# Optimization experiments

Hardware: AMD Instinct MI355X
Metric: run time of the kernel (lower is better)

The kernel has to match this reference:

```python
import jax, jax.numpy as jnp
import numpy as np

# Static problem dims (match input_specs)
B, N, C, H, W = 1, 3, 128, 256, 256
HEADS = 4
# _compute_dynamic_scales(256,256) with max_attention_size=4096:
# min_scale = max(2, int(sqrt(65536/4096))) = 4 -> scales [4,8,16], sorted desc:
SCALES = [16, 8, 4]


def setup_inputs() -> dict:
    key = jax.random.key(0)
    ks = jax.random.split(key, 8)
    S = len(SCALES)
    std = 0.05  # small init to keep logits in a sane range
    return {
        "query": jax.random.normal(ks[0], (B, C, H, W), jnp.float32),
        "keys": jax.random.normal(ks[1], (B, N, C, H, W), jnp.float32),
        "values": jax.random.normal(ks[2], (B, N, C, H, W), jnp.float32),
        "wq": jax.random.normal(ks[3], (S, C, C), jnp.float32) * std,
        "bq": jnp.zeros((S, C), jnp.float32),
        "wk": jax.random.normal(ks[4], (S, C, C), jnp.float32) * std,
        "bk": jnp.zeros((S, C), jnp.float32),
        "wv": jax.random.normal(ks[5], (S, C, C), jnp.float32) * std,
        "bv": jnp.zeros((S, C), jnp.float32),
        "fusion_w": jax.random.normal(ks[6], (C, 3 * C), jnp.float32) * std,
        "fusion_b": jnp.zeros((C,), jnp.float32),
        "out_w": jax.random.normal(ks[7], (C, C), jnp.float32) * std,
        "out_b": jnp.zeros((C,), jnp.float32),
    }


def _pool(x, s):
    """Average pool by integer factor s over the last two dims (adaptive_avg_pool2d
    with divisible sizes)."""
    *lead, c, h, w = x.shape
    return x.reshape(*lead, c, h // s, s, w // s, s).mean(axis=(-3, -1))


def _conv1x1(x, w, b):
    # x: [..., C_in, H, W], w: [C_out, C_in], b: [C_out]
    y = jnp.einsum('...chw,oc->...ohw', x, w)
    return y + b.reshape((1,) * (y.ndim - 3) + (-1, 1, 1))


def reference(query, keys, values, wq, bq, wk, bk, wv, bv,
              fusion_w, fusion_b, out_w, out_b):
    hd = C // HEADS
    outs = []
    for si, s in enumerate(SCALES):
        Hs, Ws = H // s, W // s
        L = Hs * Ws
        q_s = _pool(query, s)   # [B,C,Hs,Ws]
        k_s = _pool(keys, s)    # [B,N,C,Hs,Ws]
        v_s = _pool(values, s)  # [B,N,C,Hs,Ws]
        q = _conv1x1(q_s, wq[si], bq[si])
        k = _conv1x1(k_s, wk[si], bk[si])
        v = _conv1x1(v_s, wv[si], bv[si])
        q = q.reshape(B, HEADS, hd, L).transpose(0, 1, 3, 2)       # [B,h,L,d]
        k = k.reshape(B, N, HEADS, hd, L)                          # [B,N,h,d,M]
        v = v.reshape(B, N, HEADS, hd, L).transpose(0, 1, 2, 4, 3) # [B,N,h,M,d]
        scores = jnp.einsum('bhld,bnhdm->bnhlm', q, k) * (hd ** -0.5)
        attn = jax.nn.softmax(scores, axis=-1)                      # stable softmax
        out = jnp.einsum('bnhlm,bnhmd->bnhld', attn, v).mean(axis=1)  # mean over anchors
        out = out.transpose(0, 1, 3, 2).reshape(B, C, Hs, Ws)
        if s > 1:
            # F.interpolate bilinear, align_corners=False (half-pixel centers)
            out = jax.image.resize(out, (B, C, H, W), method='bilinear')
        outs.append(out)
    fused = jnp.concatenate(outs, axis=1)  # [B, 3C, H, W]
    y = _conv1x1(fused, fusion_w, fusion_b)
    return _conv1x1(y, out_w, out_b)
```

## Files before the change

### kernel.cpp

```cpp
#include <hip/hip_runtime.h>
#include <hip/hip_bf16.h>


typedef __attribute__((ext_vector_type(8))) short bf16x8;
typedef __attribute__((ext_vector_type(4))) float f32x4;

__device__ inline ushort rne_bf16(float x) {
  uint u = __float_as_uint(x);
  return (ushort)((u + 0x7fffu + ((u >> 16) & 1u)) >> 16);
}

__device__ inline uint pk2_bf16(float a, float b) {
  float2 f2; f2.x = a; f2.y = b;
  __hip_bfloat162 h = __float22bfloat162_rn(f2);
  union { __hip_bfloat162 h; uint u; } cvt; cvt.h = h;
  return cvt.u;
}

__global__ __launch_bounds__(256) void pool4_kernel(
    const float* __restrict__ query, const float* __restrict__ keys,
    const float* __restrict__ values, float* __restrict__ out)
{
  int idx = blockIdx.x * 256 + threadIdx.x;
  int x = idx & 63, y = (idx >> 6) & 63, mc = idx >> 12;
  int map = mc >> 7, c = mc & 127;
  const float* src;
  if (map == 0)      src = query  + (size_t)c * 65536;
  else if (map <= 3) src = keys   + (size_t)((map - 1) * 128 + c) * 65536;
  else               src = values + (size_t)((map - 4) * 128 + c) * 65536;
  src += (y * 4) * 256 + x * 4;
  float s = 0.f;
#pragma unroll
  for (int r = 0; r < 4; ++r) {
    float4 v = *(const float4*)(src + r * 256);
    s += v.x + v.y + v.z + v.w;
  }
  out[idx] = s * 0.0625f;
}

__global__ __launch_bounds__(256) void pool2_kernel(
    const float* __restrict__ in, float* __restrict__ out, int hw)
{
  int idx = blockIdx.x * 256 + threadIdx.x;
  int x = idx % hw; int y = (idx / hw) % hw; int mc = idx / (hw * hw);
  int w2 = hw * 2;
  const float* s = in + (size_t)mc * w2 * w2 + (2 * y) * w2 + 2 * x;
  float2 a = *(const float2*)s;
  float2 b = *(const float2*)(s + w2);
  out[idx] = (a.x + a.y + b.x + b.y) * 0.25f;
}

__global__ __launch_bounds__(256) void precomp_kernel(
    const float* __restrict__ fusion_w, const float* __restrict__ fusion_b,
    const float* __restrict__ out_w, const float* __restrict__ out_b,
    float* __restrict__ Wc, float* __restrict__ bc)
{
  int idx = blockIdx.x * 256 + threadIdx.x;
  if (idx < 128 * 384) {
    int o = idx / 384, k = idx % 384;
    float s = 0.f;
    for (int c = 0; c < 128; ++c)
      s = fmaf(out_w[o * 128 + c], fusion_w[c * 384 + k], s);
    Wc[idx] = s;
  } else if (idx < 128 * 384 + 128) {
    int o = idx - 128 * 384;
    float s = out_b[o];
    for (int c = 0; c < 128; ++c)
      s = fmaf(out_w[o * 128 + c], fusion_b[c], s);
    bc[o] = s;
  }
}

__global__ __launch_bounds__(256) void proj_kernel(
    const float* __restrict__ pooled,
    ushort* __restrict__ qb, ushort* __restrict__ kbb, ushort* __restrict__ vbb,
    const float* __restrict__ wq, const float* __restrict__ bq,
    const float* __restrict__ wk, const float* __restrict__ bk,
    const float* __restrict__ wv, const float* __restrict__ bv,
    int si, int L, float qscale)
{
  __shared__ float Wt[32][68];
  __shared__ float Xs[32][64];
  int map = blockIdx.z;
  int o0 = blockIdx.y * 64;
  int l0 = blockIdx.x * 64;
  const float* w; const float* b; float sc = 1.f;
  if (map == 0)      { w = wq + si * 16384; b = bq + si * 128; sc = qscale; }
  else if (map <= 3) { w = wk + si * 16384; b = bk + si * 128; }
  else               { w = wv + si * 16384; b = bv + si * 128; }
  const float* src = pooled + (size_t)map * 128 * L;
  int t = threadIdx.x;
  int og = t >> 4, lg = t & 15;
  float acc[4][4] = {};
  for (int c0 = 0; c0 < 128; c0 += 32) {
    __syncthreads();
    {
      int o = t >> 2, ci = (t & 3) * 8;
      const float* wp = w + (o0 + o) * 128 + c0 + ci;
      float4 a = *(const float4*)wp, d = *(const float4*)(wp + 4);
      Wt[ci + 0][o] = a.x; Wt[ci + 1][o] = a.y; Wt[ci + 2][o] = a.z; Wt[ci + 3][o] = a.w;
      Wt[ci + 4][o] = d.x; Wt[ci + 5][o] = d.y; Wt[ci + 6][o] = d.z; Wt[ci + 7][o] = d.w;
    }
    {
      int c = t >> 3, li = (t & 7) * 8;
      const float* xp = src + (size_t)(c0 + c) * L + l0 + li;
      float4 a = *(const float4*)xp, d = *(const float4*)(xp + 4);
      *(float4*)&Xs[c][li] = a; *(float4*)&Xs[c][li + 4] = d;
    }
    __syncthreads();
#pragma unroll 8
    for (int k = 0; k < 32; ++k) {
      float4 wv4 = *(const float4*)&Wt[k][4 * og];
      float4 xv4 = *(const float4*)&Xs[k][4 * lg];
      float wa[4] = {wv4.x, wv4.y, wv4.z, wv4.w};
      float xa[4] = {xv4.x, xv4.y, xv4.z, xv4.w};
#pragma unroll
      for (int r = 0; r < 4; ++r)
#pragma unroll
        for (int c = 0; c < 4; ++c)
          acc[r][c] = fmaf(wa[r], xa[c], acc[r][c]);
    }
  }
  float4 b4 = *(const float4*)&b[o0 + 4 * og];
  float ba[4] = {b4.x, b4.y, b4.z, b4.w};
  if (map < 4) {
    ushort* dst = (map == 0) ? qb : (kbb + (size_t)(map - 1) * L * 32 * 4);
    int o4 = o0 + 4 * og;
    size_t hbase = (size_t)(o4 >> 5) * L * 32 + (o4 & 31);
#pragma unroll
    for (int li = 0; li < 4; ++li) {
      ushort4 r;
      r.x = rne_bf16((acc[0][li] + ba[0]) * sc);
      r.y = rne_bf16((acc[1][li] + ba[1]) * sc);
      r.z = rne_bf16((acc[2][li] + ba[2]) * sc);
      r.w = rne_bf16((acc[3][li] + ba[3]) * sc);
      *(ushort4*)&dst[hbase + (size_t)(l0 + 4 * lg + li) * 32] = r;
    }
  } else {
    ushort* dst = vbb + (size_t)(map - 4) * 128 * L;
    int m = l0 + 4 * lg;
#pragma unroll
    for (int oi = 0; oi < 4; ++oi) {
      int o = o0 + 4 * og + oi;
      int h = o >> 5, d = o & 31;
      ushort4 r;
      r.x = rne_bf16(acc[oi][0] + ba[oi]);
      r.y = rne_bf16(acc[oi][1] + ba[oi]);
      r.z = rne_bf16(acc[oi][2] + ba[oi]);
      r.w = rne_bf16(acc[oi][3] + ba[oi]);
      size_t off = (size_t)h * 32 * L
                 + ((size_t)(m >> 5) * 2 + (d >> 4)) * 512
                 + (size_t)(d & 15) * 32 + ((m >> 3) & 3) * 8 + (m & 7);
      *(ushort4*)&dst[off] = r;
    }
  }
}

#define PSTR 72
__global__ __launch_bounds__(256, 4) void attn_mfma_kernel(
    const ushort* __restrict__ qb, const ushort* __restrict__ kb,
    const ushort* __restrict__ vb, float* __restrict__ onp,
    float* __restrict__ lsp, int L, int msplit)
{
  __shared__ __align__(16) ushort P[2][4][2][16][PSTR];
  int t = threadIdx.x;
  int wave = t >> 6, lane = t & 63;
  int col = lane & 15, quad = lane >> 4;
  int head = blockIdx.y;
  int anchor = blockIdx.z / msplit, mpart = blockIdx.z % msplit;
  int l = blockIdx.x * 128 + wave * 32;
  int mlen = L / msplit, mbase = mpart * mlen;
  int ntile = mlen >> 6;

  const ushort* qh = qb + (size_t)head * L * 32;
  const ushort* kh = kb + ((size_t)anchor * 4 + head) * L * 32;
  const ushort* vh = vb + ((size_t)anchor * 4 + head) * 32 * L;

  bf16x8 qfA = *(const bf16x8*)(qh + (size_t)(l + col) * 32 + quad * 8);
  bf16x8 qfB = *(const bf16x8*)(qh + (size_t)(l + 16 + col) * 32 + quad * 8);
  const ushort* kbase = kh + (size_t)mbase * 32 + col * 32 + quad * 8;
  const ushort* vbase = vh + (size_t)(mbase >> 5) * 1024 + col * 32 + quad * 8;

  f32x4 odA0 = {0.f,0.f,0.f,0.f}, odA1 = {0.f,0.f,0.f,0.f};
  f32x4 odB0 = {0.f,0.f,0.f,0.f}, odB1 = {0.f,0.f,0.f,0.f};
  f32x4 lsaA = {0.f,0.f,0.f,0.f}, lsaB = {0.f,0.f,0.f,0.f};
  const f32x4 z = {0.f,0.f,0.f,0.f};
  const bf16x8 ones = {16256,16256,16256,16256,16256,16256,16256,16256};

  ushort* Pa = &P[0][wave][0][0][0];
  ushort* Pb = &P[1][wave][0][0][0];
  const int HOF = 16 * PSTR;

  auto expstore = [&](f32x4 a0, f32x4 a1, f32x4 a2, f32x4 a3, ushort* Pw) {
    float sv[4][4] = {{a0.x,a0.y,a0.z,a0.w},{a1.x,a1.y,a1.z,a1.w},
                      {a2.x,a2.y,a2.z,a2.w},{a3.x,a3.y,a3.z,a3.w}};
#pragma unroll
    for (int j = 0; j < 4; ++j) {
      uint u0 = pk2_bf16(__builtin_amdgcn_exp2f(sv[j][0]),
                         __builtin_amdgcn_exp2f(sv[j][1]));
      uint u1 = pk2_bf16(__builtin_amdgcn_exp2f(sv[j][2]),
                         __builtin_amdgcn_exp2f(sv[j][3]));
      uint2 dw; dw.x = u0; dw.y = u1;
      *(uint2*)&Pw[col * PSTR + 16 * j + quad * 4] = dw;
    }
  };

  bf16x8 k0 = *(const bf16x8*)(kbase);
  bf16x8 k1 = *(const bf16x8*)(kbase + 512);
  bf16x8 k2 = *(const bf16x8*)(kbase + 1024);
  bf16x8 k3 = *(const bf16x8*)(kbase + 1536);
  {
    f32x4 t0 = __builtin_amdgcn_mfma_f32_16x16x32_bf16(k0, qfA, z, 0, 0, 0);
    f32x4 t1 = __builtin_amdgcn_mfma_f32_16x16x32_bf16(k1, qfA, z, 0, 0, 0);
    f32x4 t2 = __builtin_amdgcn_mfma_f32_16x16x32_bf16(k2, qfA, z, 0, 0, 0);
    f32x4 t3 = __builtin_amdgcn_mfma_f32_16x16x32_bf16(k3, qfA, z, 0, 0, 0);
    expstore(t0, t1, t2, t3, Pa);
    t0 = __builtin_amdgcn_mfma_f32_16x16x32_bf16(k0, qfB, z, 0, 0, 0);
    t1 = __builtin_amdgcn_mfma_f32_16x16x32_bf16(k1, qfB, z, 0, 0, 0);
    t2 = __builtin_amdgcn_mfma_f32_16x16x32_bf16(k2, qfB, z, 0, 0, 0);
    t3 = __builtin_amdgcn_mfma_f32_16x16x32_bf16(k3, qfB, z, 0, 0, 0);
    const ushort* kp1 = kbase + ((ntile > 1) ? 64 * 32 : 0);
    k0 = *(const bf16x8*)(kp1);
    k1 = *(const bf16x8*)(kp1 + 512);
    k2 = *(const bf16x8*)(kp1 + 1024);
    k3 = *(const bf16x8*)(kp1 + 1536);
    expstore(t0, t1, t2, t3, Pa + HOF);
  }

  for (int i = 1; i < ntile; ++i) {
    const ushort* vpn = vbase + (i - 1) * 2048;
    bf16x8 vA = *(const bf16x8*)(vpn);
    bf16x8 vB = *(const bf16x8*)(vpn + 1024);
    bf16x8 vC = *(const bf16x8*)(vpn + 512);
    bf16x8 vD = *(const bf16x8*)(vpn + 1536);
    bf16x8 pA0 = *(const bf16x8*)(&Pa[col * PSTR + quad * 8]);
    bf16x8 pA1 = *(const bf16x8*)(&Pa[col * PSTR + 32 + quad * 8]);
    bf16x8 pB0 = *(const bf16x8*)(&Pa[HOF + col * PSTR + quad * 8]);
    bf16x8 pB1 = *(const bf16x8*)(&Pa[HOF + col * PSTR + 32 + quad * 8]);
    f32x4 t0 = __builtin_amdgcn_mfma_f32_16x16x32_bf16(k0, qfA, z, 0, 0, 0);
    f32x4 t1 = __builtin_amdgcn_mfma_f32_16x16x32_bf16(k1, qfA, z, 0, 0, 0);
    f32x4 t2 = __builtin_amdgcn_mfma_f32_16x16x32_bf16(k2, qfA, z, 0, 0, 0);
    f32x4 t3 = __builtin_amdgcn_mfma_f32_16x16x32_bf16(k3, qfA, z, 0, 0, 0);
    lsaA = __builtin_amdgcn_mfma_f32_16x16x32_bf16(pA0, ones, lsaA, 0, 0, 0);
    lsaA = __builtin_amdgcn_mfma_f32_16x16x32_bf16(pA1, ones, lsaA, 0, 0, 0);
    odA0 = __builtin_amdgcn_mfma_f32_16x16x32_bf16(pA0, vA, odA0, 0, 0, 0);
    odA0 = __builtin_amdgcn_mfma_f32_16x16x32_bf16(pA1, vB, odA0, 0, 0, 0);
    odA1 = __builtin_amdgcn_mfma_f32_16x16x32_bf16(pA0, vC, odA1, 0, 0, 0);
    odA1 = __builtin_amdgcn_mfma_f32_16x16x32_bf16(pA1, vD, odA1, 0, 0, 0);
    expstore(t0, t1, t2, t3, Pb);
    t0 = __builtin_amdgcn_mfma_f32_16x16x32_bf16(k0, qfB, z, 0, 0, 0);
    t1 = __builtin_amdgcn_mfma_f32_16x16x32_bf16(k1, qfB, z, 0, 0, 0);
    t2 = __builtin_amdgcn_mfma_f32_16x16x32_bf16(k2, qfB, z, 0, 0, 0);
    t3 = __builtin_amdgcn_mfma_f32_16x16x32_bf16(k3, qfB, z, 0, 0, 0);
    {
      const ushort* kpn = kbase + ((i + 1 < ntile) ? (i + 1) * 2048 : 0);
      k0 = *(const bf16x8*)(kpn);
      k1 = *(const bf16x8*)(kpn + 512);
      k2 = *(const bf16x8*)(kpn + 1024);
      k3 = *(const bf16x8*)(kpn + 1536);
    }
    lsaB = __builtin_amdgcn_mfma_f32_16x16x32_bf16(pB0, ones, lsaB, 0, 0, 0);
    lsaB = __builtin_amdgcn_mfma_f32_16x16x32_bf16(pB1, ones, lsaB, 0, 0, 0);
    odB0 = __builtin_amdgcn_mfma_f32_16x16x32_bf16(pB0, vA, odB0, 0, 0, 0);
    odB0 = __builtin_amdgcn_mfma_f32_16x16x32_bf16(pB1, vB, odB0, 0, 0, 0);
    odB1 = __builtin_amdgcn_mfma_f32_16x16x32_bf16(pB0, vC, odB1, 0, 0, 0);
    odB1 = __builtin_amdgcn_mfma_f32_16x16x32_bf16(pB1, vD, odB1, 0, 0, 0);
    expstore(t0, t1, t2, t3, Pb + HOF);
    ushort* tp = Pa; Pa = Pb; Pb = tp;
  }

  {
    const ushort* vpe = vbase + (ntile - 1) * 2048;
    bf16x8 vA = *(const bf16x8*)(vpe);
    bf16x8 vB = *(const bf16x8*)(vpe + 1024);
    bf16x8 vC = *(const bf16x8*)(vpe + 512);
    bf16x8 vD = *(const bf16x8*)(vpe + 1536);
    bf16x8 pA0 = *(const bf16x8*)(&Pa[col * PSTR + quad * 8]);
    bf16x8 pA1 = *(const bf16x8*)(&Pa[col * PSTR + 32 + quad * 8]);
    bf16x8 pB0 = *(const bf16x8*)(&Pa[HOF + col * PSTR + quad * 8]);
    bf16x8 pB1 = *(const bf16x8*)(&Pa[HOF + col * PSTR + 32 + quad * 8]);
    lsaA = __builtin_amdgcn_mfma_f32_16x16x32_bf16(pA0, ones, lsaA, 0, 0, 0);
    lsaA = __builtin_amdgcn_mfma_f32_16x16x32_bf16(pA1, ones, lsaA, 0, 0, 0);
    odA0 = __builtin_amdgcn_mfma_f32_16x16x32_bf16(pA0, vA, odA0, 0, 0, 0);
    odA0 = __builtin_amdgcn_mfma_f32_16x16x32_bf16(pA1, vB, odA0, 0, 0, 0);
    odA1 = __builtin_amdgcn_mfma_f32_16x16x32_bf16(pA0, vC, odA1, 0, 0, 0);
    odA1 = __builtin_amdgcn_mfma_f32_16x16x32_bf16(pA1, vD, odA1, 0, 0, 0);
    lsaB = __builtin_amdgcn_mfma_f32_16x16x32_bf16(pB0, ones, lsaB, 0, 0, 0);
    lsaB = __builtin_amdgcn_mfma_f32_16x16x32_bf16(pB1, ones, lsaB, 0, 0, 0);
    odB0 = __builtin_amdgcn_mfma_f32_16x16x32_bf16(pB0, vA, odB0, 0, 0, 0);
    odB0 = __builtin_amdgcn_mfma_f32_16x16x32_bf16(pB1, vB, odB0, 0, 0, 0);
    odB1 = __builtin_amdgcn_mfma_f32_16x16x32_bf16(pB0, vC, odB1, 0, 0, 0);
    odB1 = __builtin_amdgcn_mfma_f32_16x16x32_bf16(pB1, vD, odB1, 0, 0, 0);
  }

  float* on2 = onp + ((size_t)(mpart * 3 + anchor) * 128 + (size_t)(head * 32)) * L;
  float* ls2 = lsp + ((size_t)(mpart * 3 + anchor) * 4 + head) * L;
  if (col == 0) {
    *(f32x4*)&ls2[l + quad * 4] = lsaA;
    *(f32x4*)&ls2[l + 16 + quad * 4] = lsaB;
  }
  *(f32x4*)&on2[(size_t)col * L + l + quad * 4]             = odA0;
  *(f32x4*)&on2[(size_t)(16 + col) * L + l + quad * 4]      = odA1;
  *(f32x4*)&on2[(size_t)col * L + l + 16 + quad * 4]        = odB0;
  *(f32x4*)&on2[(size_t)(16 + col) * L + l + 16 + quad * 4] = odB1;
}

__global__ __launch_bounds__(256) void norm_kernel(
    const float* __restrict__ on4,  const float* __restrict__ ls4,  float* __restrict__ a4,
    const float* __restrict__ on8,  const float* __restrict__ ls8,  float* __restrict__ a8,
    const float* __restrict__ on16, const float* __restrict__ ls16, float* __restrict__ a16)
{
  int i = blockIdx.x * 256 + threadIdx.x;
  const float* on; const float* ls; float* ax; int L;
  if (i < 131072)      { on = on4;  ls = ls4;  ax = a4;  L = 4096; }
  else if (i < 163840) { i -= 131072; on = on8;  ls = ls8;  ax = a8;  L = 1024; }
  else                 { i -= 163840; on = on16; ls = ls16; ax = a16; L = 256; }
  int e = i * 4;
  int c = e / L, l = e % L;
  int h = c >> 5;
  float ax0 = 0.f, ax1 = 0.f, ax2 = 0.f, ax3 = 0.f;
  for (int a = 0; a < 3; ++a) {
    float n0 = 0.f, n1 = 0.f, n2 = 0.f, n3 = 0.f;
    float d0 = 0.f, d1 = 0.f, d2 = 0.f, d3 = 0.f;
#pragma unroll
    for (int mp = 0; mp < 2; ++mp) {
      int g = mp * 3 + a;
      float4 o = *(const float4*)&on[((size_t)g * 128 + c) * L + l];
      float4 s = *(const float4*)&ls[((size_t)g * 4 + h) * L + l];
      n0 += o.x; n1 += o.y; n2 += o.z; n3 += o.w;
      d0 += s.x; d1 += s.y; d2 += s.z; d3 += s.w;
    }
    ax0 += n0 / d0; ax1 += n1 / d1; ax2 += n2 / d2; ax3 += n3 / d3;
  }
  const float third = 1.f / 3.f;
  float4 r = make_float4(ax0 * third, ax1 * third, ax2 * third, ax3 * third);
  *(float4*)&ax[e] = r;
}

__global__ __launch_bounds__(256) void ygemm_kernel(
    const float* __restrict__ a16, const float* __restrict__ a8,
    const float* __restrict__ a4, const float* __restrict__ Wc,
    float* __restrict__ y16, float* __restrict__ y8, float* __restrict__ y4)
{
  __shared__ float Wt[32][68];
  __shared__ float Xs[32][64];
  int bx = blockIdx.x;
  int o0 = blockIdx.y * 64;
  int sci; int lt; const float* src; float* dst; int L;
  if (bx < 4)       { sci = 0; lt = bx;      src = a16; dst = y16; L = 256; }
  else if (bx < 20) { sci = 1; lt = bx - 4;  src = a8;  dst = y8;  L = 1024; }
  else              { sci = 2; lt = bx - 20; src = a4;  dst = y4;  L = 4096; }
  int l0 = lt * 64;
  int coff = sci * 128;
  int t = threadIdx.x;
  int og = t >> 4, lg = t & 15;
  float acc[4][4] = {};
  for (int c0 = 0; c0 < 128; c0 += 32) {
    __syncthreads();
    {
      int o = t >> 2, ci = (t & 3) * 8;
      const float* wp = Wc + (o0 + o) * 384 + coff + c0 + ci;
      float4 a = *(const float4*)wp, d = *(const float4*)(wp + 4);
      Wt[ci + 0][o] = a.x; Wt[ci + 1][o] = a.y; Wt[ci + 2][o] = a.z; Wt[ci + 3][o] = a.w;
      Wt[ci + 4][o] = d.x; Wt[ci + 5][o] = d.y; Wt[ci + 6][o] = d.z; Wt[ci + 7][o] = d.w;
    }
    {
      int c = t >> 3, li = (t & 7) * 8;
      const float* xp = src + (size_t)(c0 + c) * L + l0 + li;
      float4 a = *(const float4*)xp, d = *(const float4*)(xp + 4);
      *(float4*)&Xs[c][li] = a; *(float4*)&Xs[c][li + 4] = d;
    }
    __syncthreads();
#pragma unroll 8
    for (int k = 0; k < 32; ++k) {
      float4 wv4 = *(const float4*)&Wt[k][4 * og];
      float4 xv4 = *(const float4*)&Xs[k][4 * lg];
      float wa[4] = {wv4.x, wv4.y, wv4.z, wv4.w};
      float xa[4] = {xv4.x, xv4.y, xv4.z, xv4.w};
#pragma unroll
      for (int r = 0; r < 4; ++r)
#pragma unroll
        for (int c = 0; c < 4; ++c)
          acc[r][c] = fmaf(wa[r], xa[c], acc[r][c]);
    }
  }
#pragma unroll
  for (int r = 0; r < 4; ++r) {
    float4 v = make_float4(acc[r][0], acc[r][1], acc[r][2], acc[r][3]);
    *(float4*)&dst[(size_t)(o0 + 4 * og + r) * L + l0 + 4 * lg] = v;
  }
}

__device__ inline void add_bilinear(const float* __restrict__ Yrow0,
                                    const float* __restrict__ Yrow1,
                                    int ssz, float sf, float fy,
                                    int px0, float* r)
{
#pragma unroll
  for (int j = 0; j < 4; ++j) {
    float sx = (px0 + j + 0.5f) * sf - 0.5f;
    int xi = (int)floorf(sx);
    float fx = sx - xi;
    int x0 = max(xi, 0), x1 = min(xi + 1, ssz - 1);
    float a0 = Yrow0[x0], a1 = Yrow0[x1];
    float b0 = Yrow1[x0], b1 = Yrow1[x1];
    float v0 = a0 + fx * (a1 - a0);
    float v1 = b0 + fx * (b1 - b0);
    r[j] += v0 + fy * (v1 - v0);
  }
}

__global__ __launch_bounds__(256) void upsample_kernel(
    const float* __restrict__ y16, const float* __restrict__ y8,
    const float* __restrict__ y4, const float* __restrict__ bc,
    float* __restrict__ outp)
{
  int idx = blockIdx.x * 256 + threadIdx.x;
  int x4 = idx & 63, py = (idx >> 6) & 255, o = idx >> 14;
  int px0 = x4 * 4;
  float b = bc[o];
  float r[4] = {b, b, b, b};
#pragma unroll
  for (int s = 0; s < 3; ++s) {
    const float* Y; int ssz; float sf;
    if (s == 0)      { Y = y16; ssz = 16; sf = 1.f / 16.f; }
    else if (s == 1) { Y = y8;  ssz = 32; sf = 1.f / 8.f; }
    else             { Y = y4;  ssz = 64; sf = 1.f / 4.f; }
    const float* Yo = Y + (size_t)o * ssz * ssz;
    float sy = (py + 0.5f) * sf - 0.5f;
    int yi = (int)floorf(sy);
    float fy = sy - yi;
    int yy0 = max(yi, 0), yy1 = min(yi + 1, ssz - 1);
    add_bilinear(Yo + yy0 * ssz, Yo + yy1 * ssz, ssz, sf, fy, px0, r);
  }
  float4 v = make_float4(r[0], r[1], r[2], r[3]);
  *(float4*)&outp[(size_t)o * 65536 + py * 256 + px0] = v;
}

extern "C" void kernel_launch(void* const* d_in, const int* in_sizes, int n_in,
                              void* d_out, int out_size, void* d_ws, size_t ws_size,
                              hipStream_t stream) {
  const float* query    = (const float*)d_in[0];
  const float* keys     = (const float*)d_in[1];
  const float* values   = (const float*)d_in[2];
  const float* wq       = (const float*)d_in[3];
  const float* bq       = (const float*)d_in[4];
  const float* wk       = (const float*)d_in[5];
  const float* bk       = (const float*)d_in[6];
  const float* wv       = (const float*)d_in[7];
  const float* bv       = (const float*)d_in[8];
  const float* fusion_w = (const float*)d_in[9];
  const float* fusion_b = (const float*)d_in[10];
  const float* out_w    = (const float*)d_in[11];
  const float* out_b    = (const float*)d_in[12];
  float* wsf  = (float*)d_ws;
  float* outp = (float*)d_out;

  const size_t P4   = 0;
  const size_t P8   = 3670016;
  const size_t P16  = 4587520;
  const size_t ONP4  = 0;
  const size_t LSP4  = 3145728;
  const size_t ONP8  = 3244032;
  const size_t LSP8  = 4030464;
  const size_t ONP16 = 4055040;
  const size_t LSP16 = 4448256;
  const size_t Y4   = 0;
  const size_t Y8   = 524288;
  const size_t Y16  = 655360;
  const size_t QB4  = 4816896;
  const size_t KB4  = 5079040;
  const size_t VB4  = 5865472;
  const size_t QB8  = 6651904;
  const size_t KB8  = 6717440;
  const size_t VB8  = 6914048;
  const size_t QB16 = 7110656;
  const size_t KB16 = 7127040;
  const size_t VB16 = 7176192;
  const size_t A4   = 7225344;
  const size_t A8   = 7749632;
  const size_t A16  = 7880704;
  const size_t WC   = 7913472;
  const size_t BC   = 7962624;

  precomp_kernel<<<(128*384 + 128 + 255) / 256, 256, 0, stream>>>(
      fusion_w, fusion_b, out_w, out_b, wsf + WC, wsf + BC);
  pool4_kernel<<<7*128*4096/256, 256, 0, stream>>>(query, keys, values, wsf + P4);
  pool2_kernel<<<7*128*1024/256, 256, 0, stream>>>(wsf + P4, wsf + P8, 32);
  pool2_kernel<<<7*128*256/256,  256, 0, stream>>>(wsf + P8, wsf + P16, 16);

  const float qsc = 0.17677669529663687f * 1.4426950408889634f;
  proj_kernel<<<dim3(64, 2, 7), 256, 0, stream>>>(wsf + P4,
      (ushort*)(wsf + QB4), (ushort*)(wsf + KB4), (ushort*)(wsf + VB4),
      wq, bq, wk, bk, wv, bv, 2, 4096, qsc);
  proj_kernel<<<dim3(16, 2, 7), 256, 0, stream>>>(wsf + P8,
      (ushort*)(wsf + QB8), (ushort*)(wsf + KB8), (ushort*)(wsf + VB8),
      wq, bq, wk, bk, wv, bv, 1, 1024, qsc);
  proj_kernel<<<dim3(4, 2, 7), 256, 0, stream>>>(wsf + P16,
      (ushort*)(wsf + QB16), (ushort*)(wsf + KB16), (ushort*)(wsf + VB16),
      wq, bq, wk, bk, wv, bv, 0, 256, qsc);

  attn_mfma_kernel<<<dim3(32, 4, 6), 256, 0, stream>>>(
      (const ushort*)(wsf + QB4), (const ushort*)(wsf + KB4),
      (const ushort*)(wsf + VB4), wsf + ONP4, wsf + LSP4, 4096, 2);
  attn_mfma_kernel<<<dim3(8, 4, 6), 256, 0, stream>>>(
      (const ushort*)(wsf + QB8), (const ushort*)(wsf + KB8),
      (const ushort*)(wsf + VB8), wsf + ONP8, wsf + LSP8, 1024, 2);
  attn_mfma_kernel<<<dim3(2, 4, 6), 256, 0, stream>>>(
      (const ushort*)(wsf + QB16), (const ushort*)(wsf + KB16),
      (const ushort*)(wsf + VB16), wsf + ONP16, wsf + LSP16, 256, 2);

  norm_kernel<<<672, 256, 0, stream>>>(
      wsf + ONP4, wsf + LSP4, wsf + A4,
      wsf + ONP8, wsf + LSP8, wsf + A8,
      wsf + ONP16, wsf + LSP16, wsf + A16);

  ygemm_kernel<<<dim3(84, 2), 256, 0, stream>>>(
      wsf + A16, wsf + A8, wsf + A4, wsf + WC,
      wsf + Y16, wsf + Y8, wsf + Y4);
  upsample_kernel<<<8192, 256, 0, stream>>>(
      wsf + Y16, wsf + Y8, wsf + Y4, wsf + BC, outp);
}
```

Measured before the change: 414.1 us.

## Fuse three pooling levels into one kernel using wave shuffles

Replaces the 4x pooling kernel and the two 2x pooling kernels with one kernel where each thread averages a 16x4 strip into four 4x4-pooled outputs. It then uses lane shuffles to form the 8x and 16x pooled values. This removes two launches and the re-reading of intermediate pooled maps from memory. In exchange it has fewer threads, each doing more loads, and the row-strided access pattern may lower memory parallelism.

```diff
diff --git a/kernel.cpp b/kernel.cpp
--- a/kernel.cpp
+++ b/kernel.cpp
@@ -17,37 +17,63 @@
   return cvt.u;
 }
 
-__global__ __launch_bounds__(256) void pool4_kernel(
+__global__ __launch_bounds__(256) void pool_fused_kernel(
     const float* __restrict__ query, const float* __restrict__ keys,
-    const float* __restrict__ values, float* __restrict__ out)
+    const float* __restrict__ values, float* __restrict__ out4,
+    float* __restrict__ out8, float* __restrict__ out16)
 {
   int idx = blockIdx.x * 256 + threadIdx.x;
-  int x = idx & 63, y = (idx >> 6) & 63, mc = idx >> 12;
+  int x = idx & 63;
+  int t = (idx >> 6) & 15;
+  int mc = idx >> 10;
   int map = mc >> 7, c = mc & 127;
   const float* src;
   if (map == 0)      src = query  + (size_t)c * 65536;
   else if (map <= 3) src = keys   + (size_t)((map - 1) * 128 + c) * 65536;
   else               src = values + (size_t)((map - 4) * 128 + c) * 65536;
-  src += (y * 4) * 256 + x * 4;
-  float s = 0.f;
-#pragma unroll
-  for (int r = 0; r < 4; ++r) {
-    float4 v = *(const float4*)(src + r * 256);
-    s += v.x + v.y + v.z + v.w;
-  }
-  out[idx] = s * 0.0625f;
-}
-
-__global__ __launch_bounds__(256) void pool2_kernel(
-    const float* __restrict__ in, float* __restrict__ out, int hw)
-{
-  int idx = blockIdx.x * 256 + threadIdx.x;
-  int x = idx % hw; int y = (idx / hw) % hw; int mc = idx / (hw * hw);
-  int w2 = hw * 2;
-  const float* s = in + (size_t)mc * w2 * w2 + (2 * y) * w2 + 2 * x;
-  float2 a = *(const float2*)s;
-  float2 b = *(const float2*)(s + w2);
-  out[idx] = (a.x + a.y + b.x + b.y) * 0.25f;
+  src += (t * 16) * 256 + x * 4;
+
+  float4 v0  = *(const float4*)(src + 0 * 256);
+  float4 v1  = *(const float4*)(src + 1 * 256);
+  float4 v2  = *(const float4*)(src + 2 * 256);
+  float4 v3  = *(const float4*)(src + 3 * 256);
+  float4 v4  = *(const float4*)(src + 4 * 256);
+  float4 v5  = *(const float4*)(src + 5 * 256);
+  float4 v6  = *(const float4*)(src + 6 * 256);
+  float4 v7  = *(const float4*)(src + 7 * 256);
+  float4 v8  = *(const float4*)(src + 8 * 256);
+  float4 v9  = *(const float4*)(src + 9 * 256);
+  float4 v10 = *(const float4*)(src + 10 * 256);
+  float4 v11 = *(const float4*)(src + 11 * 256);
+  float4 v12 = *(const float4*)(src + 12 * 256);
+  float4 v13 = *(const float4*)(src + 13 * 256);
+  float4 v14 = *(const float4*)(src + 14 * 256);
+  float4 v15 = *(const float4*)(src + 15 * 256);
+
+  float s0 = ((v0.x + v0.y + v0.z + v0.w) + (v1.x + v1.y + v1.z + v1.w)
+            + (v2.x + v2.y + v2.z + v2.w) + (v3.x + v3.y + v3.z + v3.w)) * 0.0625f;
+  float s1 = ((v4.x + v4.y + v4.z + v4.w) + (v5.x + v5.y + v5.z + v5.w)
+            + (v6.x + v6.y + v6.z + v6.w) + (v7.x + v7.y + v7.z + v7.w)) * 0.0625f;
+  float s2 = ((v8.x + v8.y + v8.z + v8.w) + (v9.x + v9.y + v9.z + v9.w)
+            + (v10.x + v10.y + v10.z + v10.w) + (v11.x + v11.y + v11.z + v11.w)) * 0.0625f;
+  float s3 = ((v12.x + v12.y + v12.z + v12.w) + (v13.x + v13.y + v13.z + v13.w)
+            + (v14.x + v14.y + v14.z + v14.w) + (v15.x + v15.y + v15.z + v15.w)) * 0.0625f;
+
+  float* o4 = out4 + (size_t)mc * 4096 + (t * 4) * 64 + x;
+  o4[0] = s0; o4[64] = s1; o4[128] = s2; o4[192] = s3;
+
+  float s0p = __shfl_xor(s0, 1), s1p = __shfl_xor(s1, 1);
+  float s2p = __shfl_xor(s2, 1), s3p = __shfl_xor(s3, 1);
+  float e0 = ((s0 + s0p) + s1 + s1p) * 0.25f;
+  float e1 = ((s2 + s2p) + s3 + s3p) * 0.25f;
+  float e0q = __shfl_xor(e0, 2), e1q = __shfl_xor(e1, 2);
+  float p16 = ((e0 + e0q) + e1 + e1q) * 0.25f;
+  if ((x & 1) == 0) {
+    float* o8 = out8 + (size_t)mc * 1024 + (t * 2) * 32 + (x >> 1);
+    o8[0] = e0; o8[32] = e1;
+  }
+  if ((x & 3) == 0)
+    out16[(size_t)mc * 256 + t * 16 + (x >> 2)] = p16;
 }
 
 __global__ __launch_bounds__(256) void precomp_kernel(
@@ -485,9 +511,8 @@
 
   precomp_kernel<<<(128*384 + 128 + 255) / 256, 256, 0, stream>>>(
       fusion_w, fusion_b, out_w, out_b, wsf + WC, wsf + BC);
-  pool4_kernel<<<7*128*4096/256, 256, 0, stream>>>(query, keys, values, wsf + P4);
-  pool2_kernel<<<7*128*1024/256, 256, 0, stream>>>(wsf + P4, wsf + P8, 32);
-  pool2_kernel<<<7*128*256/256,  256, 0, stream>>>(wsf + P8, wsf + P16, 16);
+  pool_fused_kernel<<<3584, 256, 0, stream>>>(
+      query, keys, values, wsf + P4, wsf + P8, wsf + P16);
 
   const float qsc = 0.17677669529663687f * 1.4426950408889634f;
   proj_kernel<<<dim3(64, 2, 7), 256, 0, stream>>>(wsf + P4,
```

Result: no change. 415.1 us (+0.3%).
